# Kernel tuning notes

Hardware: AMD Instinct MI355X
Metric: run time of the kernel (lower is better)

Reference implementation:

```python
import jax, jax.numpy as jnp
import numpy as np

D = 1024
H = 16
HD = D // H
FF = 4096
B, N = 8, 1024


def setup_inputs() -> dict:
    key = jax.random.key(0)
    ks = jax.random.split(key, 12)
    s = lambda fan_in: 1.0 / np.sqrt(fan_in)
    return {
        "x": jax.random.normal(ks[0], (B, N, D), dtype=jnp.float32),
        "ln1_g": jnp.ones((D,), jnp.float32),
        "ln1_b": jnp.zeros((D,), jnp.float32),
        "ln2_g": jnp.ones((D,), jnp.float32),
        "ln2_b": jnp.zeros((D,), jnp.float32),
        "W_qkv": jax.random.uniform(ks[1], (3 * D, D), jnp.float32, -s(D), s(D)),
        "b_qkv": jax.random.uniform(ks[2], (3 * D,), jnp.float32, -s(D), s(D)),
        "W_proj": jax.random.uniform(ks[3], (D, D), jnp.float32, -s(D), s(D)),
        "b_proj": jax.random.uniform(ks[4], (D,), jnp.float32, -s(D), s(D)),
        "W1": jax.random.uniform(ks[5], (FF, D), jnp.float32, -s(D), s(D)),
        "b1": jax.random.uniform(ks[6], (FF,), jnp.float32, -s(D), s(D)),
        "W2": jax.random.uniform(ks[7], (D, FF), jnp.float32, -s(FF), s(FF)),
        "b2": jax.random.uniform(ks[8], (D,), jnp.float32, -s(FF), s(FF)),
    }


def _layernorm(x, g, b, eps=1e-5):
    mu = jnp.mean(x, axis=-1, keepdims=True)
    var = jnp.mean(jnp.square(x - mu), axis=-1, keepdims=True)
    return (x - mu) * jax.lax.rsqrt(var + eps) * g + b


def _gelu(x):
    return jax.nn.gelu(x, approximate=False)  # torch nn.GELU default (erf)


def _forward(x, ln1_g, ln1_b, ln2_g, ln2_b, W_qkv, b_qkv, W_proj, b_proj, W1, b1, W2, b2):
    b, n, d = x.shape
    h = _layernorm(x, ln1_g, ln1_b)
    qkv = h @ W_qkv.T + b_qkv                      # [B,N,3D]
    qkv = qkv.reshape(b, n, 3, H, HD).transpose(2, 0, 3, 1, 4)  # [3,B,H,N,HD]
    q, k, v = qkv[0], qkv[1], qkv[2]
    scores = jnp.einsum("bhqd,bhkd->bhqk", q, k) / np.sqrt(HD)
    attn = jax.nn.softmax(scores, axis=-1)
    ctx = jnp.einsum("bhqk,bhkd->bhqd", attn, v)   # [B,H,N,HD]
    ctx = ctx.transpose(0, 2, 1, 3).reshape(b, n, d)
    attn_out = ctx @ W_proj.T + b_proj
    out = attn_out + x                              # residual 1
    skip = out
    hh = _layernorm(out, ln2_g, ln2_b)
    hh = _gelu(hh @ W1.T + b1)
    hh = _gelu(hh @ W2.T + b2)                      # note: final GELU per source
    return hh + skip


def reference(x, ln1_g, ln1_b, ln2_g, ln2_b, W_qkv, b_qkv, W_proj, b_proj, W1, b1, W2, b2):
    return _forward(x, ln1_g, ln1_b, ln2_g, ln2_b, W_qkv, b_qkv, W_proj, b_proj, W1, b1, W2, b2)
```

## Files before the change

### kernel.cpp

```cpp
#include <hip/hip_runtime.h>


typedef unsigned short ushort_t;
typedef __bf16 bf16x8 __attribute__((ext_vector_type(8)));
typedef float f32x4 __attribute__((ext_vector_type(4)));
typedef unsigned short u16x8 __attribute__((ext_vector_type(8)));

__device__ __forceinline__ void async_ld16(const void* g, void* l) {
  __builtin_amdgcn_global_load_lds(
      (void __attribute__((address_space(1)))*)const_cast<void*>(g),
      (void __attribute__((address_space(3)))*)l, 16, 0, 0);
}

__device__ __forceinline__ float bf2f(ushort_t h) {
  union { unsigned int u; float f; } v;
  v.u = ((unsigned int)h) << 16;
  return v.f;
}
__device__ __forceinline__ ushort_t f2bf(float f) {
  union { float f; unsigned int u; } v;
  v.f = f;
  unsigned int r = v.u + 0x7FFFu + ((v.u >> 16) & 1u);
  return (ushort_t)(r >> 16);
}
__device__ __forceinline__ float fast_exp2(float x) {
#if __has_builtin(__builtin_amdgcn_exp2f)
  return __builtin_amdgcn_exp2f(x);
#else
  return __expf(x * 0.6931471805599453f);
#endif
}
__device__ __forceinline__ float gelu_f(float x) {
  float y = 0.7978845608028654f * (x + 0.044715f * x * x * x);
  float e = __expf(2.0f * y);
  float t = 1.0f - 2.0f / (e + 1.0f);
  return 0.5f * x * (1.0f + t);
}

__global__ void __launch_bounds__(256) cvt_f32_bf16(const float* __restrict__ src,
                                                    ushort_t* __restrict__ dst, int n) {
  int i = (blockIdx.x * 256 + threadIdx.x) * 8;
  if (i >= n) return;
  float4 a = *(const float4*)(src + i);
  float4 b = *(const float4*)(src + i + 4);
  u16x8 o;
  o[0] = f2bf(a.x); o[1] = f2bf(a.y); o[2] = f2bf(a.z); o[3] = f2bf(a.w);
  o[4] = f2bf(b.x); o[5] = f2bf(b.y); o[6] = f2bf(b.z); o[7] = f2bf(b.w);
  *(u16x8*)(dst + i) = o;
}

__global__ void __launch_bounds__(256) cvt_f32_bf16_2(const float* __restrict__ s0,
                                                      ushort_t* __restrict__ d0, int n0,
                                                      const float* __restrict__ s1,
                                                      ushort_t* __restrict__ d1, int n1) {
  int i = (blockIdx.x * 256 + threadIdx.x) * 8;
  const float* src;
  ushort_t* dst;
  if (i < n0) {
    src = s0 + i; dst = d0 + i;
  } else {
    int j = i - n0;
    if (j >= n1) return;
    src = s1 + j; dst = d1 + j;
  }
  float4 a = *(const float4*)(src);
  float4 b = *(const float4*)(src + 4);
  u16x8 o;
  o[0] = f2bf(a.x); o[1] = f2bf(a.y); o[2] = f2bf(a.z); o[3] = f2bf(a.w);
  o[4] = f2bf(b.x); o[5] = f2bf(b.y); o[6] = f2bf(b.z); o[7] = f2bf(b.w);
  *(u16x8*)dst = o;
}

__global__ void __launch_bounds__(256) ln_f32(const float* __restrict__ X,
                                              const float* __restrict__ G,
                                              const float* __restrict__ Bb,
                                              ushort_t* __restrict__ Y) {
  int tok = blockIdx.x * 4 + (threadIdx.x >> 6);
  int lane = threadIdx.x & 63;
  const float* xr = X + (size_t)tok * 1024 + lane * 16;
  float v[16];
#pragma unroll
  for (int c = 0; c < 4; c++) {
    float4 a = *(const float4*)(xr + c * 4);
    v[c * 4 + 0] = a.x; v[c * 4 + 1] = a.y; v[c * 4 + 2] = a.z; v[c * 4 + 3] = a.w;
  }
  float s = 0.f, ss = 0.f;
#pragma unroll
  for (int j = 0; j < 16; j++) { s += v[j]; ss += v[j] * v[j]; }
#pragma unroll
  for (int off = 32; off >= 1; off >>= 1) {
    s += __shfl_xor(s, off);
    ss += __shfl_xor(ss, off);
  }
  float mu = s * (1.f / 1024.f);
  float var = ss * (1.f / 1024.f) - mu * mu;
  float rs = rsqrtf(var + 1e-5f);
  u16x8 o0, o1;
#pragma unroll
  for (int c = 0; c < 4; c++) {
    float4 g = *(const float4*)(G + lane * 16 + c * 4);
    float4 bb = *(const float4*)(Bb + lane * 16 + c * 4);
    ushort_t* op = (c < 2) ? (ushort_t*)&o0 : (ushort_t*)&o1;
    int base = (c & 1) * 4;
    op[base + 0] = f2bf((v[c * 4 + 0] - mu) * rs * g.x + bb.x);
    op[base + 1] = f2bf((v[c * 4 + 1] - mu) * rs * g.y + bb.y);
    op[base + 2] = f2bf((v[c * 4 + 2] - mu) * rs * g.z + bb.z);
    op[base + 3] = f2bf((v[c * 4 + 3] - mu) * rs * g.w + bb.w);
  }
  ushort_t* yr = Y + (size_t)tok * 1024 + lane * 16;
  *(u16x8*)yr = o0;
  *(u16x8*)(yr + 8) = o1;
}

__global__ void __launch_bounds__(256) ln_bf16(const ushort_t* __restrict__ X,
                                               const float* __restrict__ G,
                                               const float* __restrict__ Bb,
                                               ushort_t* __restrict__ Y) {
  int tok = blockIdx.x * 4 + (threadIdx.x >> 6);
  int lane = threadIdx.x & 63;
  const ushort_t* xr = X + (size_t)tok * 1024 + lane * 16;
  u16x8 x0 = *(const u16x8*)xr;
  u16x8 x1 = *(const u16x8*)(xr + 8);
  float v[16];
  float s = 0.f, ss = 0.f;
#pragma unroll
  for (int j = 0; j < 8; j++) { v[j] = bf2f(x0[j]); v[8 + j] = bf2f(x1[j]); }
#pragma unroll
  for (int j = 0; j < 16; j++) { s += v[j]; ss += v[j] * v[j]; }
#pragma unroll
  for (int off = 32; off >= 1; off >>= 1) {
    s += __shfl_xor(s, off);
    ss += __shfl_xor(ss, off);
  }
  float mu = s * (1.f / 1024.f);
  float var = ss * (1.f / 1024.f) - mu * mu;
  float rs = rsqrtf(var + 1e-5f);
  u16x8 o0, o1;
#pragma unroll
  for (int c = 0; c < 4; c++) {
    float4 g = *(const float4*)(G + lane * 16 + c * 4);
    float4 bb = *(const float4*)(Bb + lane * 16 + c * 4);
    ushort_t* op = (c < 2) ? (ushort_t*)&o0 : (ushort_t*)&o1;
    int base = (c & 1) * 4;
    op[base + 0] = f2bf((v[c * 4 + 0] - mu) * rs * g.x + bb.x);
    op[base + 1] = f2bf((v[c * 4 + 1] - mu) * rs * g.y + bb.y);
    op[base + 2] = f2bf((v[c * 4 + 2] - mu) * rs * g.z + bb.z);
    op[base + 3] = f2bf((v[c * 4 + 3] - mu) * rs * g.w + bb.w);
  }
  ushort_t* yr = Y + (size_t)tok * 1024 + lane * 16;
  *(u16x8*)yr = o0;
  *(u16x8*)(yr + 8) = o1;
}

template <int BK>
__global__ void __launch_bounds__(256, (BK == 64 ? 4 : 2))
gemm_bt(const ushort_t* __restrict__ A,
        const ushort_t* __restrict__ Bw,
        const float* __restrict__ bias,
        const float* __restrict__ ResF,
        const ushort_t* __restrict__ ResB,
        ushort_t* __restrict__ Cb,
        float* __restrict__ Cf,
        int M, int N, int K, int act, int swz) {
  constexpr int NG = BK / 8;
  constexpr int GM = NG - 1;
  constexpr int RPP = 2048 / BK;
  constexpr int NP = BK / 16;
  constexpr int NC = BK / 32;
  __shared__ __align__(16) ushort_t sAB[2 * 128 * BK];
  ushort_t* sA = sAB;
  ushort_t* sB = sAB + 128 * BK;
  int t = threadIdx.x;
  int wave = t >> 6, lane = t & 63;
  int quad = lane >> 4, l16 = lane & 15;
  int wm = (wave & 1) * 64, wn = (wave >> 1) * 64;

  int bx = blockIdx.x, by = blockIdx.y;
  if (swz) {
    int lid = by * gridDim.x + bx;
    int xcd = lid & 7, slot = lid >> 3;
    int mchunk = gridDim.y >> 3;
    by = xcd * mchunk + slot / gridDim.x;
    bx = slot % gridDim.x;
  }
  int m0 = by * 128, n0 = bx * 128;

  f32x4 zero = {0.f, 0.f, 0.f, 0.f};
  f32x4 acc[4][4];
#pragma unroll
  for (int i = 0; i < 4; i++)
#pragma unroll
    for (int j = 0; j < 4; j++) acc[i][j] = zero;

  int srow = t / NG;
  int scol = ((t & GM) ^ (srow & GM)) * 8;
  const ushort_t* gA = A + (size_t)(m0 + srow) * K + scol;
  const ushort_t* gB = Bw + (size_t)(n0 + srow) * K + scol;

  for (int k0 = 0; k0 < K; k0 += BK) {
#pragma unroll
    for (int p = 0; p < NP; p++) {
      async_ld16(gA + (size_t)p * RPP * K + k0, sA + p * 2048 + wave * 512);
      async_ld16(gB + (size_t)p * RPP * K + k0, sB + p * 2048 + wave * 512);
    }
    __syncthreads();
#pragma unroll
    for (int c = 0; c < NC; c++) {
      int col = (((c * 4 + quad) ^ (l16 & GM)) * 8);
      bf16x8 af[4], bfr[4];
#pragma unroll
      for (int i = 0; i < 4; i++) {
        af[i]  = *(const bf16x8*)(sA + (wm + i * 16 + l16) * BK + col);
        bfr[i] = *(const bf16x8*)(sB + (wn + i * 16 + l16) * BK + col);
      }
#pragma unroll
      for (int mi = 0; mi < 4; mi++)
#pragma unroll
        for (int ni = 0; ni < 4; ni++)
          acc[mi][ni] = __builtin_amdgcn_mfma_f32_16x16x32_bf16(af[mi], bfr[ni], acc[mi][ni], 0, 0, 0);
    }
    __syncthreads();
  }

  float bv[4];
#pragma unroll
  for (int ni = 0; ni < 4; ni++) bv[ni] = bias[n0 + wn + ni * 16 + l16];

  if (Cf) {
#pragma unroll
    for (int mi = 0; mi < 4; mi++) {
      int row = m0 + wm + mi * 16 + quad * 4;
#pragma unroll
      for (int ni = 0; ni < 4; ni++) {
        int col = n0 + wn + ni * 16 + l16;
#pragma unroll
        for (int r = 0; r < 4; r++) {
          size_t idx = (size_t)(row + r) * N + col;
          float vv = acc[mi][ni][r] + bv[ni];
          if (act) vv = gelu_f(vv);
          if (ResB) vv += bf2f(ResB[idx]);
          Cf[idx] = vv;
        }
      }
    }
  } else {
    ushort_t* eb = sAB + wave * (16 * 72);
    int lr = lane >> 2, lc = (lane & 3) * 8;
#pragma unroll
    for (int mi = 0; mi < 4; mi++) {
      int row = m0 + wm + mi * 16;
#pragma unroll
      for (int ni = 0; ni < 4; ni++)
#pragma unroll
        for (int r = 0; r < 4; r++) {
          float vv = acc[mi][ni][r] + bv[ni];
          if (act) vv = gelu_f(vv);
          eb[(quad * 4 + r) * 72 + ni * 16 + l16] = f2bf(vv);
        }
#pragma unroll
      for (int hc = 0; hc < 64; hc += 32) {
        u16x8 o = *(const u16x8*)(eb + lr * 72 + hc + lc);
        size_t gidx = (size_t)(row + lr) * N + n0 + wn + hc + lc;
        if (ResF) {
          float4 ra = *(const float4*)(ResF + gidx);
          float4 rb = *(const float4*)(ResF + gidx + 4);
          u16x8 o2;
          o2[0] = f2bf(bf2f(o[0]) + ra.x); o2[1] = f2bf(bf2f(o[1]) + ra.y);
          o2[2] = f2bf(bf2f(o[2]) + ra.z); o2[3] = f2bf(bf2f(o[3]) + ra.w);
          o2[4] = f2bf(bf2f(o[4]) + rb.x); o2[5] = f2bf(bf2f(o[5]) + rb.y);
          o2[6] = f2bf(bf2f(o[6]) + rb.z); o2[7] = f2bf(bf2f(o[7]) + rb.w);
          *(u16x8*)(Cb + gidx) = o2;
        } else {
          *(u16x8*)(Cb + gidx) = o;
        }
      }
    }
  }
}

__global__ void __launch_bounds__(256) vtrans(const ushort_t* __restrict__ qkv,
                                              ushort_t* __restrict__ Vt) {
  __shared__ ushort_t tile[64][72];
  int t = threadIdx.x;
  int bh = blockIdx.y;
  int b = bh >> 4, h = bh & 15;
  int n0 = blockIdx.x * 64;
  int r = t >> 3;
  int c8 = (t & 7) * 8;
  const ushort_t* src = qkv + ((size_t)(b * 1024 + n0)) * 3072 + 2048 + h * 64;
#pragma unroll
  for (int rr = r; rr < 64; rr += 32) {
    u16x8 d = *(const u16x8*)(src + (size_t)rr * 3072 + c8);
#pragma unroll
    for (int j = 0; j < 8; j++) tile[rr][c8 + j] = d[j];
  }
  __syncthreads();
#pragma unroll
  for (int hh = r; hh < 64; hh += 32) {
    u16x8 o;
#pragma unroll
    for (int j = 0; j < 8; j++) o[j] = tile[c8 + j][hh];
    *(u16x8*)(Vt + ((size_t)bh * 64 + hh) * 1024 + n0 + c8) = o;
  }
}

__global__ void __launch_bounds__(256) attn_kernel(const ushort_t* __restrict__ qkv,
                                                   const ushort_t* __restrict__ Vt,
                                                   ushort_t* __restrict__ ctx) {
  __shared__ __align__(16) ushort_t sK[128 * 64];
  __shared__ __align__(16) ushort_t sV[64 * 128];
  __shared__ __align__(16) ushort_t sP[4 * 16 * 152];
  int t = threadIdx.x, wave = t >> 6, lane = t & 63;
  int quad = lane >> 4, l16 = lane & 15;
  int bh = blockIdx.y, b = bh >> 4, h = bh & 15;
  int q0 = blockIdx.x * 64 + wave * 16;
  size_t tokbase = (size_t)b * 1024;
  const float SC2 = 0.18033688011112042f;

  const ushort_t* qrow = qkv + (tokbase + q0 + l16) * 3072 + h * 64;
  bf16x8 qf0 = *(const bf16x8*)(qrow + quad * 8);
  bf16x8 qf1 = *(const bf16x8*)(qrow + 32 + quad * 8);

  f32x4 zero = {0.f, 0.f, 0.f, 0.f};
  f32x4 O[4];
#pragma unroll
  for (int i = 0; i < 4; i++) O[i] = zero;
  float m2 = -3.0e38f, l = 0.f;

  int kvlK = wave * 32 + (lane >> 3);
  int hdKx = lane & 7;
  ushort_t* pw = sP + wave * (16 * 152);

  for (int kv0 = 0; kv0 < 1024; kv0 += 128) {
#pragma unroll
    for (int j = 0; j < 4; j++) {
      int kvl = kvlK + j * 8;
      int hd = (hdKx ^ (kvl & 7)) * 8;
      async_ld16(qkv + (tokbase + kv0 + kvl) * 3072 + 1024 + h * 64 + hd,
                 sK + wave * 2048 + j * 512);
      int hdv = wave * 16 + j * 4 + (lane >> 4);
      int kvloc = ((lane & 15) ^ (hdv & 15)) * 8;
      async_ld16(Vt + ((size_t)bh * 64 + hdv) * 1024 + kv0 + kvloc,
                 sV + wave * 2048 + j * 512);
    }
    __syncthreads();

    f32x4 st[8];
    __builtin_amdgcn_s_setprio(1);
#pragma unroll
    for (int s = 0; s < 8; s++) {
      bf16x8 kf0 = *(const bf16x8*)(sK + (s * 16 + l16) * 64 + ((quad ^ (l16 & 7)) * 8));
      bf16x8 kf1 = *(const bf16x8*)(sK + (s * 16 + l16) * 64 + (((4 + quad) ^ (l16 & 7)) * 8));
      st[s] = __builtin_amdgcn_mfma_f32_16x16x32_bf16(kf0, qf0, zero, 0, 0, 0);
      st[s] = __builtin_amdgcn_mfma_f32_16x16x32_bf16(kf1, qf1, st[s], 0, 0, 0);
    }
    __builtin_amdgcn_s_setprio(0);
    f32x4 mx4 = st[0];
#pragma unroll
    for (int s = 1; s < 8; s++)
#pragma unroll
      for (int r = 0; r < 4; r++) mx4[r] = fmaxf(mx4[r], st[s][r]);
    float mx = fmaxf(fmaxf(mx4[0], mx4[1]), fmaxf(mx4[2], mx4[3]));
    mx = fmaxf(mx, __shfl_xor(mx, 16));
    mx = fmaxf(mx, __shfl_xor(mx, 32));
    float mx2 = mx * SC2;
    if (!__all(mx2 - m2 <= 8.0f)) {
      float mnew2 = fmaxf(m2, mx2);
      float alpha = fast_exp2(m2 - mnew2);
      m2 = mnew2;
      l *= alpha;
#pragma unroll
      for (int ti = 0; ti < 4; ti++)
#pragma unroll
        for (int r = 0; r < 4; r++) O[ti][r] *= alpha;
    }
    float rs = 0.f;
#pragma unroll
    for (int s = 0; s < 8; s++)
#pragma unroll
      for (int r = 0; r < 4; r++) {
        st[s][r] = fast_exp2(fmaf(st[s][r], SC2, -m2));
        rs += st[s][r];
      }
    rs += __shfl_xor(rs, 16);
    rs += __shfl_xor(rs, 32);
    l += rs;
#pragma unroll
    for (int s = 0; s < 8; s++) {
      uint2 pk;
      pk.x = __builtin_amdgcn_perm(__float_as_uint(st[s][1]), __float_as_uint(st[s][0]), 0x07060302u);
      pk.y = __builtin_amdgcn_perm(__float_as_uint(st[s][3]), __float_as_uint(st[s][2]), 0x07060302u);
      *(uint2*)(pw + l16 * 152 + s * 16 + quad * 4) = pk;
    }
    __builtin_amdgcn_s_setprio(1);
#pragma unroll
    for (int c = 0; c < 4; c++) {
      bf16x8 pf = *(const bf16x8*)(pw + l16 * 152 + c * 32 + quad * 8);
#pragma unroll
      for (int ti = 0; ti < 4; ti++) {
        bf16x8 vf = *(const bf16x8*)(sV + (ti * 16 + l16) * 128 + (((c * 4 + quad) ^ l16) * 8));
        O[ti] = __builtin_amdgcn_mfma_f32_16x16x32_bf16(vf, pf, O[ti], 0, 0, 0);
      }
    }
    __builtin_amdgcn_s_setprio(0);
    __syncthreads();
  }
  float inv = 1.0f / l;
  ushort_t* cb = ctx + (tokbase + q0 + l16) * 1024 + h * 64;
#pragma unroll
  for (int ti = 0; ti < 4; ti++) {
    uint2 pk;
    pk.x = (unsigned int)f2bf(O[ti][0] * inv) | ((unsigned int)f2bf(O[ti][1] * inv) << 16);
    pk.y = (unsigned int)f2bf(O[ti][2] * inv) | ((unsigned int)f2bf(O[ti][3] * inv) << 16);
    *(uint2*)(cb + ti * 16 + quad * 4) = pk;
  }
}

extern "C" void kernel_launch(void* const* d_in, const int* in_sizes, int n_in,
                              void* d_out, int out_size, void* d_ws, size_t ws_size,
                              hipStream_t stream) {
  (void)in_sizes; (void)n_in; (void)out_size; (void)ws_size;
  const float* x     = (const float*)d_in[0];
  const float* ln1g  = (const float*)d_in[1];
  const float* ln1b  = (const float*)d_in[2];
  const float* ln2g  = (const float*)d_in[3];
  const float* ln2b  = (const float*)d_in[4];
  const float* Wqkv  = (const float*)d_in[5];
  const float* bqkv  = (const float*)d_in[6];
  const float* Wproj = (const float*)d_in[7];
  const float* bproj = (const float*)d_in[8];
  const float* W1    = (const float*)d_in[9];
  const float* b1    = (const float*)d_in[10];
  const float* W2    = (const float*)d_in[11];
  const float* b2    = (const float*)d_in[12];
  float* out = (float*)d_out;
  char* ws = (char*)d_ws;
  const size_t MB = 1u << 20;
  ushort_t* Wqkv_b  = (ushort_t*)(ws + 0);
  ushort_t* Wproj_b = (ushort_t*)(ws + 6 * MB);
  ushort_t* h1      = (ushort_t*)(ws + 8 * MB);
  ushort_t* qkv     = (ushort_t*)(ws + 24 * MB);
  ushort_t* Vt      = (ushort_t*)(ws + 72 * MB);
  ushort_t* ctx     = (ushort_t*)(ws + 8 * MB);
  ushort_t* out1    = (ushort_t*)(ws + 24 * MB);
  ushort_t* W1_b    = (ushort_t*)(ws + 0);
  ushort_t* h2      = (ushort_t*)(ws + 8 * MB);
  ushort_t* ff1     = (ushort_t*)(ws + 40 * MB);
  ushort_t* W2_b    = (ushort_t*)(ws + 0);

  cvt_f32_bf16_2<<<2048, 256, 0, stream>>>(Wqkv, Wqkv_b, 3 * 1024 * 1024,
                                           Wproj, Wproj_b, 1024 * 1024);
  ln_f32<<<2048, 256, 0, stream>>>(x, ln1g, ln1b, h1);
  gemm_bt<64><<<dim3(24, 64), 256, 0, stream>>>(h1, Wqkv_b, bqkv, nullptr, nullptr, qkv, nullptr, 8192, 3072, 1024, 0, 0);
  vtrans<<<dim3(16, 128), 256, 0, stream>>>(qkv, Vt);
  attn_kernel<<<dim3(16, 128), 256, 0, stream>>>(qkv, Vt, ctx);
  gemm_bt<128><<<dim3(8, 64), 256, 0, stream>>>(ctx, Wproj_b, bproj, x, nullptr, out1, nullptr, 8192, 1024, 1024, 0, 0);
  cvt_f32_bf16<<<2048, 256, 0, stream>>>(W1, W1_b, 4 * 1024 * 1024);
  ln_bf16<<<2048, 256, 0, stream>>>(out1, ln2g, ln2b, h2);
  gemm_bt<64><<<dim3(32, 64), 256, 0, stream>>>(h2, W1_b, b1, nullptr, nullptr, ff1, nullptr, 8192, 4096, 1024, 1, 0);
  cvt_f32_bf16<<<2048, 256, 0, stream>>>(W2, W2_b, 4 * 1024 * 1024);
  gemm_bt<128><<<dim3(8, 64), 256, 0, stream>>>(ff1, W2_b, b2, nullptr, out1, nullptr, out, 8192, 1024, 4096, 1, 1);
}
```

Measured before the change: 476.9 us.

## Add 256x256-tile 8-wave pipelined GEMM for QKV and FFN1 projections

Introduces a new GEMM kernel with 256x256 output tiles, 512 threads, XOR-swizzled LDS, and a double-buffered schedule. The global-to-LDS loads are interleaved with MFMA phases and the MFMA sections run at raised wave priority. It replaces the 128-tile gemm_bt for the QKV and W1 projections, raising arithmetic intensity per loaded byte and hiding load latency. In exchange it uses more LDS and registers per block, and the grid is smaller (384/512 blocks), which may cause tail effects on the CUs.

Result: slower. 492.1 us (+3.2%).

```diff
diff --git a/kernel.cpp b/kernel.cpp
--- a/kernel.cpp
+++ b/kernel.cpp
@@ -150,6 +150,132 @@
   ushort_t* yr = Y + (size_t)tok * 1024 + lane * 16;
   *(u16x8*)yr = o0;
   *(u16x8*)(yr + 8) = o1;
+}
+
+#define MF16 __builtin_amdgcn_mfma_f32_16x16x32_bf16
+#define STG_A(BUF, R0, KK) \
+  async_ld16(gA + (size_t)((R0) + srow_l) * K + (KK) + scol_l, sA + (BUF)*16384 + ((R0) + ldsrow) * 64)
+#define STG_B(BUF, R0, KK) \
+  async_ld16(gB + (size_t)((R0) + srow_l) * K + (KK) + scol_l, sB + (BUF)*16384 + ((R0) + ldsrow) * 64)
+#define PHASE(MQ, SOFF, READB, STAGE_STMT, DO_VM)                                                    \
+  {                                                                                                  \
+    if (READB) {                                                                                     \
+      _Pragma("unroll") for (int ni = 0; ni < 4; ni++) {                                             \
+        int br = wc * 64 + ni * 16 + l16;                                                            \
+        bfr[ni][0] = *(const bf16x8*)(sB + (SOFF) + br * 64 + ((quad ^ (l16 & 7)) * 8));             \
+        bfr[ni][1] = *(const bf16x8*)(sB + (SOFF) + br * 64 + (((4 + quad) ^ (l16 & 7)) * 8));       \
+      }                                                                                              \
+    }                                                                                                \
+    int ar = wr * 128 + (MQ) * 32 + l16;                                                             \
+    bf16x8 a00 = *(const bf16x8*)(sA + (SOFF) + ar * 64 + ((quad ^ (l16 & 7)) * 8));                 \
+    bf16x8 a01 = *(const bf16x8*)(sA + (SOFF) + ar * 64 + (((4 + quad) ^ (l16 & 7)) * 8));           \
+    bf16x8 a10 = *(const bf16x8*)(sA + (SOFF) + (ar + 16) * 64 + ((quad ^ (l16 & 7)) * 8));          \
+    bf16x8 a11 = *(const bf16x8*)(sA + (SOFF) + (ar + 16) * 64 + (((4 + quad) ^ (l16 & 7)) * 8));    \
+    STAGE_STMT;                                                                                      \
+    __builtin_amdgcn_sched_barrier(0);                                                               \
+    if (DO_VM) asm volatile("s_waitcnt vmcnt(6)" ::: "memory");                                      \
+    __builtin_amdgcn_s_barrier();                                                                    \
+    __builtin_amdgcn_s_setprio(1);                                                                   \
+    _Pragma("unroll") for (int ni = 0; ni < 4; ni++) {                                               \
+      acc[(MQ)*2 + 0][ni] = MF16(a00, bfr[ni][0], acc[(MQ)*2 + 0][ni], 0, 0, 0);                     \
+      acc[(MQ)*2 + 0][ni] = MF16(a01, bfr[ni][1], acc[(MQ)*2 + 0][ni], 0, 0, 0);                     \
+      acc[(MQ)*2 + 1][ni] = MF16(a10, bfr[ni][0], acc[(MQ)*2 + 1][ni], 0, 0, 0);                     \
+      acc[(MQ)*2 + 1][ni] = MF16(a11, bfr[ni][1], acc[(MQ)*2 + 1][ni], 0, 0, 0);                     \
+    }                                                                                                \
+    __builtin_amdgcn_s_setprio(0);                                                                   \
+    __builtin_amdgcn_sched_barrier(0);                                                               \
+    __builtin_amdgcn_s_barrier();                                                                    \
+  }
+
+__global__ void __launch_bounds__(512, 2)
+gemm256_bt(const ushort_t* __restrict__ A, const ushort_t* __restrict__ Bw,
+           const float* __restrict__ bias, ushort_t* __restrict__ Cb,
+           int M, int N, int K, int act) {
+  __shared__ __align__(16) ushort_t sA[2 * 256 * 64];
+  __shared__ __align__(16) ushort_t sB[2 * 256 * 64];
+  int t = threadIdx.x;
+  int wid = t >> 6, lane = t & 63;
+  int quad = lane >> 4, l16 = lane & 15;
+  int wr = wid >> 2, wc = wid & 3;
+  int m0 = blockIdx.y * 256, n0 = blockIdx.x * 256;
+
+  int srow_l = wid * 8 + (lane >> 3);
+  int scol_l = ((lane & 7) ^ ((lane >> 3) & 7)) * 8;
+  int ldsrow = wid * 8;
+  const ushort_t* gA = A + (size_t)m0 * K;
+  const ushort_t* gB = Bw + (size_t)n0 * K;
+
+  f32x4 zero = {0.f, 0.f, 0.f, 0.f};
+  f32x4 acc[8][4];
+#pragma unroll
+  for (int i = 0; i < 8; i++)
+#pragma unroll
+    for (int j = 0; j < 4; j++) acc[i][j] = zero;
+  bf16x8 bfr[4][2];
+
+  int NT = K >> 6;
+  int NITER = NT >> 1;
+
+  STG_B(0, 0, 0);  STG_B(0, 64, 0);  STG_B(0, 128, 0); STG_B(0, 192, 0);
+  STG_A(0, 0, 0);  STG_A(0, 128, 0); STG_A(0, 64, 0);  STG_A(0, 192, 0);
+  STG_B(1, 0, 64); STG_B(1, 64, 64); STG_B(1, 128, 64); STG_B(1, 192, 64);
+  STG_A(1, 0, 64); STG_A(1, 128, 64);
+  __builtin_amdgcn_sched_barrier(0);
+  asm volatile("s_waitcnt vmcnt(6)" ::: "memory");
+  __builtin_amdgcn_s_barrier();
+
+  for (int i = 0; i < NITER - 1; ++i) {
+    int kk1 = (2 * i + 1) << 6;
+    int kk2 = (2 * i + 2) << 6;
+    int kk3 = (2 * i + 3) << 6;
+    PHASE(0, 0,     true,  { STG_A(1, 64, kk1);  STG_A(1, 192, kk1); }, false)
+    PHASE(1, 0,     false, { STG_B(0, 0, kk2);   STG_B(0, 64, kk2);  }, false)
+    PHASE(2, 0,     false, { STG_B(0, 128, kk2); STG_B(0, 192, kk2); }, false)
+    PHASE(3, 0,     false, { STG_A(0, 0, kk2);   STG_A(0, 128, kk2); }, true)
+    PHASE(0, 16384, true,  { STG_A(0, 64, kk2);  STG_A(0, 192, kk2); }, false)
+    PHASE(1, 16384, false, { STG_B(1, 0, kk3);   STG_B(1, 64, kk3);  }, false)
+    PHASE(2, 16384, false, { STG_B(1, 128, kk3); STG_B(1, 192, kk3); }, false)
+    PHASE(3, 16384, false, { STG_A(1, 0, kk3);   STG_A(1, 128, kk3); }, true)
+  }
+
+  {
+    int kkL = (NT - 1) << 6;
+    STG_A(1, 64, kkL); STG_A(1, 192, kkL);
+    __builtin_amdgcn_sched_barrier(0);
+    asm volatile("s_waitcnt vmcnt(0)" ::: "memory");
+    __builtin_amdgcn_s_barrier();
+    PHASE(0, 0,     true,  {}, false)
+    PHASE(1, 0,     false, {}, false)
+    PHASE(2, 0,     false, {}, false)
+    PHASE(3, 0,     false, {}, false)
+    PHASE(0, 16384, true,  {}, false)
+    PHASE(1, 16384, false, {}, false)
+    PHASE(2, 16384, false, {}, false)
+    PHASE(3, 16384, false, {}, false)
+  }
+
+  float bv[4];
+#pragma unroll
+  for (int ni = 0; ni < 4; ni++) bv[ni] = bias[n0 + wc * 64 + ni * 16 + l16];
+  ushort_t* eb = sA + wid * (16 * 72);
+  int lr = lane >> 2, lc = (lane & 3) * 8;
+#pragma unroll
+  for (int mi = 0; mi < 8; mi++) {
+    int row = m0 + wr * 128 + mi * 16;
+#pragma unroll
+    for (int ni = 0; ni < 4; ni++)
+#pragma unroll
+      for (int r = 0; r < 4; r++) {
+        float vv = acc[mi][ni][r] + bv[ni];
+        if (act) vv = gelu_f(vv);
+        eb[(quad * 4 + r) * 72 + ni * 16 + l16] = f2bf(vv);
+      }
+#pragma unroll
+    for (int hc = 0; hc < 64; hc += 32) {
+      u16x8 o = *(const u16x8*)(eb + lr * 72 + hc + lc);
+      *(u16x8*)(Cb + (size_t)(row + lr) * N + n0 + wc * 64 + hc + lc) = o;
+    }
+  }
 }
 
 template <int BK>
@@ -451,13 +577,13 @@
   cvt_f32_bf16_2<<<2048, 256, 0, stream>>>(Wqkv, Wqkv_b, 3 * 1024 * 1024,
                                            Wproj, Wproj_b, 1024 * 1024);
   ln_f32<<<2048, 256, 0, stream>>>(x, ln1g, ln1b, h1);
-  gemm_bt<64><<<dim3(24, 64), 256, 0, stream>>>(h1, Wqkv_b, bqkv, nullptr, nullptr, qkv, nullptr, 8192, 3072, 1024, 0, 0);
+  gemm256_bt<<<dim3(12, 32), 512, 0, stream>>>(h1, Wqkv_b, bqkv, qkv, 8192, 3072, 1024, 0);
   vtrans<<<dim3(16, 128), 256, 0, stream>>>(qkv, Vt);
   attn_kernel<<<dim3(16, 128), 256, 0, stream>>>(qkv, Vt, ctx);
   gemm_bt<128><<<dim3(8, 64), 256, 0, stream>>>(ctx, Wproj_b, bproj, x, nullptr, out1, nullptr, 8192, 1024, 1024, 0, 0);
   cvt_f32_bf16<<<2048, 256, 0, stream>>>(W1, W1_b, 4 * 1024 * 1024);
   ln_bf16<<<2048, 256, 0, stream>>>(out1, ln2g, ln2b, h2);
-  gemm_bt<64><<<dim3(32, 64), 256, 0, stream>>>(h2, W1_b, b1, nullptr, nullptr, ff1, nullptr, 8192, 4096, 1024, 1, 0);
+  gemm256_bt<<<dim3(16, 32), 512, 0, stream>>>(h2, W1_b, b1, ff1, 8192, 4096, 1024, 1);
   cvt_f32_bf16<<<2048, 256, 0, stream>>>(W2, W2_b, 4 * 1024 * 1024);
   gemm_bt<128><<<dim3(8, 64), 256, 0, stream>>>(ff1, W2_b, b2, nullptr, out1, nullptr, out, 8192, 1024, 4096, 1, 1);
 }
```
